# Kernel optimization log

Hardware: AMD Instinct MI355X
Metric: run time of the kernel (lower is better)

Reference implementation:

```python
import jax, jax.numpy as jnp
import numpy as np

B, S = 32, 2048
ENC2 = 1024   # encoder_hidden*2
DEC = 1024    # decoder_hidden
ATT = 1024    # attention_hidden


def setup_inputs() -> dict:
    key = jax.random.key(0)
    ks = jax.random.split(key, 8)
    s_enc = 1.0 / np.sqrt(ENC2)
    s_dec = 1.0 / np.sqrt(DEC)
    s_e = 1.0 / np.sqrt(ATT)
    return {
        "decoder_hidden": jax.random.normal(ks[0], (B, DEC), jnp.float32),
        "encoder_outputs": jax.random.normal(ks[1], (B, S, ENC2), jnp.float32),
        "mask": jnp.ones((B, S), dtype=bool),
        "W_enc": jax.random.uniform(ks[2], (ENC2, ATT), jnp.float32, -s_enc, s_enc),
        "b_enc": jax.random.uniform(ks[3], (ATT,), jnp.float32, -s_enc, s_enc),
        "W_dec": jax.random.uniform(ks[4], (DEC, ATT), jnp.float32, -s_dec, s_dec),
        "b_dec": jax.random.uniform(ks[5], (ATT,), jnp.float32, -s_dec, s_dec),
        "w_e": jax.random.uniform(ks[6], (ATT,), jnp.float32, -s_e, s_e),
        "b_e": jax.random.uniform(ks[7], (), jnp.float32, -s_e, s_e),
    }


def reference(decoder_hidden, encoder_outputs, mask, W_enc, b_enc, W_dec, b_dec, w_e, b_e):
    # encoder_proj: (B, S, ATT)
    encoder_proj = jnp.einsum('bse,ea->bsa', encoder_outputs, W_enc) + b_enc
    # decoder_proj: (B, 1, ATT)
    decoder_proj = (decoder_hidden @ W_dec + b_dec)[:, None, :]
    # energy: (B, S) -- Linear(ATT,1) then squeeze
    energy = jnp.einsum('bsa,a->bs', jnp.tanh(encoder_proj + decoder_proj), w_e) + b_e
    energy = jnp.where(mask, energy, -jnp.inf)
    attention_weights = jax.nn.softmax(energy, axis=1)           # (B, S)
    context = jnp.einsum('bs,bse->be', attention_weights, encoder_outputs)  # (B, ENC2)
    return context, attention_weights
```

## Files before the change

### kernel.cpp

```cpp
#include <hip/hip_runtime.h>
#include <math.h>

#define S_LEN 2048
#define ENC2  1024
#define DEC_H 1024
#define ATT   1024
#define BATCH 32

typedef __attribute__((ext_vector_type(8)))  short short8;
typedef __attribute__((ext_vector_type(16))) float f32x16;

#define DP_OFF (ATT * ENC2 * 2)

__device__ __forceinline__ unsigned short f2bf(float f) {
    unsigned int u = __float_as_uint(f);
    return (unsigned short)((u + 0x7FFFu + ((u >> 16) & 1u)) >> 16);
}

__device__ __forceinline__ float tanh_fast(float x) {
    float ax = fabsf(x);
    float e = __expf(-2.0f * ax);
    float t = (1.0f - e) / (1.0f + e);
    return copysignf(t, x);
}

__global__ void k_pack(const float* __restrict__ W, unsigned short* __restrict__ P) {
    int t  = threadIdx.x;
    int kb = blockIdx.x;
    int nb = blockIdx.y * 4 + (t >> 6);
    int l  = t & 63;
    int n  = nb * 32 + (l & 31);
    int k0 = kb * 16 + ((l >> 5) * 8);
    short8 v;
#pragma unroll
    for (int j = 0; j < 8; ++j)
        v[j] = (short)f2bf(W[(size_t)(k0 + j) * ATT + n]);
    *(short8*)(P + (((size_t)kb * 32 + nb) * 64 + l) * 8) = v;
}

__global__ void k_dproj(const float* __restrict__ dec, const float* __restrict__ Wd,
                        const float* __restrict__ b_dec, const float* __restrict__ b_enc,
                        float* __restrict__ dp) {
    int n = blockIdx.x * 256 + threadIdx.x;
    int b = blockIdx.y;
    float acc = b_dec[n] + b_enc[n];
    const float* dh = dec + b * DEC_H;
#pragma unroll 16
    for (int k = 0; k < DEC_H; ++k)
        acc = fmaf(dh[k], Wd[(size_t)k * ATT + n], acc);
    dp[b * ATT + n] = acc;
}

__launch_bounds__(512, 2)
__global__ void k_energy(const float* __restrict__ enc,
                         const short* __restrict__ BP,
                         const float* __restrict__ dp,
                         const float* __restrict__ w_e,
                         const float* __restrict__ b_e,
                         const int* __restrict__ mask,
                         float* __restrict__ energy)
{
    __shared__ short As[64 * 1024];
    float* e_lds = (float*)As;

    const int tid = threadIdx.x;
    const int r0  = blockIdx.x * 64;
    const int b   = r0 >> 11;

    {
        const float* src = enc + (size_t)r0 * ENC2;
        char* smem = (char*)As;
        for (int u = tid; u < 8192; u += 512) {
            int row = u >> 7, slot = u & 127;
            const float* p = src + (size_t)row * ENC2 + slot * 8;
            float4 f0 = *(const float4*)p;
            float4 f1 = *(const float4*)(p + 4);
            short8 v;
            v[0] = (short)f2bf(f0.x); v[1] = (short)f2bf(f0.y);
            v[2] = (short)f2bf(f0.z); v[3] = (short)f2bf(f0.w);
            v[4] = (short)f2bf(f1.x); v[5] = (short)f2bf(f1.y);
            v[6] = (short)f2bf(f1.z); v[7] = (short)f2bf(f1.w);
            int dst = row * 2048 + ((slot * 16) ^ ((row & 15) << 4));
            *(short8*)(smem + dst) = v;
        }
    }
    __syncthreads();

    const int lane = tid & 63;
    const int wid  = tid >> 6;
    const int col  = lane & 31;
    const int hi   = lane >> 5;
    const int nw   = wid * 128;

    float dv[4], wv[4];
#pragma unroll
    for (int nf = 0; nf < 4; ++nf) {
        int n = nw + nf * 32 + col;
        dv[nf] = dp[b * ATT + n];
        wv[nf] = w_e[n];
    }

    f32x16 acc[2][4] = {};
    const int xr = (col & 15) << 4;
    const char* arow0 = (const char*)As + col * 2048;
    const char* arow1 = (const char*)As + (col + 32) * 2048;

    const char* bp = (const char*)BP + (size_t)(wid * 4) * 1024 + lane * 16;

    short8 b0[4], b1[4];
#pragma unroll
    for (int nf = 0; nf < 4; ++nf) b0[nf] = *(const short8*)(bp + nf * 1024);
#pragma unroll
    for (int nf = 0; nf < 4; ++nf) b1[nf] = *(const short8*)(bp + 32768 + nf * 1024);

    for (int kb = 0; kb < 64; kb += 2) {
        {
            int off = ((kb * 32 + hi * 16) ^ xr);
            short8 a0 = *(const short8*)(arow0 + off);
            short8 a1 = *(const short8*)(arow1 + off);
#pragma unroll
            for (int nf = 0; nf < 4; ++nf) {
                acc[0][nf] = __builtin_amdgcn_mfma_f32_32x32x16_bf16(a0, b0[nf], acc[0][nf], 0, 0, 0);
                acc[1][nf] = __builtin_amdgcn_mfma_f32_32x32x16_bf16(a1, b0[nf], acc[1][nf], 0, 0, 0);
            }
            const char* pf = bp + (size_t)(kb + 2 < 64 ? kb + 2 : kb) * 32768;
#pragma unroll
            for (int nf = 0; nf < 4; ++nf) b0[nf] = *(const short8*)(pf + nf * 1024);
        }
        {
            int off = (((kb + 1) * 32 + hi * 16) ^ xr);
            short8 a0 = *(const short8*)(arow0 + off);
            short8 a1 = *(const short8*)(arow1 + off);
#pragma unroll
            for (int nf = 0; nf < 4; ++nf) {
                acc[0][nf] = __builtin_amdgcn_mfma_f32_32x32x16_bf16(a0, b1[nf], acc[0][nf], 0, 0, 0);
                acc[1][nf] = __builtin_amdgcn_mfma_f32_32x32x16_bf16(a1, b1[nf], acc[1][nf], 0, 0, 0);
            }
            const char* pf = bp + (size_t)(kb + 3 < 64 ? kb + 3 : kb) * 32768;
#pragma unroll
            for (int nf = 0; nf < 4; ++nf) b1[nf] = *(const short8*)(pf + nf * 1024);
        }
    }

    float ep[32];
#pragma unroll
    for (int mf = 0; mf < 2; ++mf)
#pragma unroll
        for (int reg = 0; reg < 16; ++reg) {
            float s = 0.0f;
#pragma unroll
            for (int nf = 0; nf < 4; ++nf)
                s = fmaf(wv[nf], tanh_fast(acc[mf][nf][reg] + dv[nf]), s);
            ep[mf * 16 + reg] = s;
        }

#pragma unroll
    for (int d = 1; d < 32; d <<= 1)
#pragma unroll
        for (int j = 0; j < 32; ++j)
            ep[j] += __shfl_xor(ep[j], d, 64);

    __syncthreads();
    if (tid < 64) e_lds[tid] = 0.0f;
    __syncthreads();

    if (col == 0) {
#pragma unroll
        for (int j = 0; j < 32; ++j) {
            int reg = j & 15;
            int row = (j >> 4) * 32 + (reg & 3) + 8 * (reg >> 2) + 4 * hi;
            atomicAdd(&e_lds[row], ep[j]);
        }
    }
    __syncthreads();

    if (tid < 64) {
        int m = r0 + tid;
        float e = e_lds[tid] + b_e[0];
        if (!mask[m]) e = -INFINITY;
        energy[m] = e;
    }
}

__global__ void k_softmax(float* __restrict__ out) {
    int b = blockIdx.x, tid = threadIdx.x;
    float* ew = out + BATCH * ATT + (size_t)b * S_LEN;
    float v[8];
#pragma unroll
    for (int i = 0; i < 8; ++i) v[i] = ew[i * 256 + tid];
    float m = v[0];
#pragma unroll
    for (int i = 1; i < 8; ++i) m = fmaxf(m, v[i]);
#pragma unroll
    for (int d = 1; d < 64; d <<= 1) m = fmaxf(m, __shfl_xor(m, d, 64));
    __shared__ float red[4], red2[4];
    int w = tid >> 6;
    if ((tid & 63) == 0) red[w] = m;
    __syncthreads();
    m = fmaxf(fmaxf(red[0], red[1]), fmaxf(red[2], red[3]));
    float s = 0.0f;
#pragma unroll
    for (int i = 0; i < 8; ++i) { v[i] = __expf(v[i] - m); s += v[i]; }
#pragma unroll
    for (int d = 1; d < 64; d <<= 1) s += __shfl_xor(s, d, 64);
    if ((tid & 63) == 0) red2[w] = s;
    __syncthreads();
    s = red2[0] + red2[1] + red2[2] + red2[3];
    float inv = 1.0f / s;
#pragma unroll
    for (int i = 0; i < 8; ++i) ew[i * 256 + tid] = v[i] * inv;
    float* ctx = out + (size_t)b * ATT;
#pragma unroll
    for (int i = 0; i < 4; ++i) ctx[i * 256 + tid] = 0.0f;
}

__global__ void k_context(const float* __restrict__ enc, const float* __restrict__ wgt,
                          float* __restrict__ ctx) {
    int sx = blockIdx.x, b = blockIdx.y, tid = threadIdx.x;
    __shared__ float wsh[128];
    if (tid < 128) wsh[tid] = wgt[(size_t)b * S_LEN + sx * 128 + tid];
    __syncthreads();
    const float* ep = enc + ((size_t)b * S_LEN + sx * 128) * ENC2 + tid * 4;
    float ax = 0, ay = 0, az = 0, aw = 0;
#pragma unroll 4
    for (int s = 0; s < 128; ++s) {
        float4 e = *(const float4*)(ep + (size_t)s * ENC2);
        float w = wsh[s];
        ax = fmaf(w, e.x, ax); ay = fmaf(w, e.y, ay);
        az = fmaf(w, e.z, az); aw = fmaf(w, e.w, aw);
    }
    float* c = ctx + (size_t)b * ATT + tid * 4;
    atomicAdd(c + 0, ax); atomicAdd(c + 1, ay);
    atomicAdd(c + 2, az); atomicAdd(c + 3, aw);
}

extern "C" void kernel_launch(void* const* d_in, const int* in_sizes, int n_in,
                              void* d_out, int out_size, void* d_ws, size_t ws_size,
                              hipStream_t stream) {
    (void)in_sizes; (void)n_in; (void)out_size; (void)ws_size;
    const float* dec   = (const float*)d_in[0];
    const float* enc   = (const float*)d_in[1];
    const int*   mask  = (const int*)d_in[2];
    const float* W_enc = (const float*)d_in[3];
    const float* b_enc = (const float*)d_in[4];
    const float* W_dec = (const float*)d_in[5];
    const float* b_dec = (const float*)d_in[6];
    const float* w_e   = (const float*)d_in[7];
    const float* b_e   = (const float*)d_in[8];

    float* out = (float*)d_out;
    unsigned short* BP = (unsigned short*)d_ws;
    float* dp = (float*)((char*)d_ws + DP_OFF);
    float* energy = out + BATCH * ATT;

    k_pack<<<dim3(64, 8), 256, 0, stream>>>(W_enc, BP);
    k_dproj<<<dim3(4, 32), 256, 0, stream>>>(dec, W_dec, b_dec, b_enc, dp);
    k_energy<<<1024, 512, 0, stream>>>(enc, (const short*)BP, dp, w_e, b_e, mask, energy);
    k_softmax<<<32, 256, 0, stream>>>(out);
    k_context<<<dim3(16, 32), 256, 0, stream>>>(enc, energy, out);
}
```

Baseline: 640.8 us.

## Pipeline encoder K-chunks through double-buffered LDS in energy kernel

The energy kernel used to stage a whole 64x1024 bf16 tile in LDS before any MFMA work. Now each block handles 256 rows and streams 64x256 K-chunks through a double buffer, so the global load of the next chunk overlaps MFMAs on the current one, and the grid shrinks to 256 blocks. The decoder-projection loop is split into four independent accumulators, and the context kernel batches eight row loads before its FMAs to raise memory-level parallelism. In exchange, the energy kernel adds more barriers and runs fewer blocks, which may lower occupancy and latency hiding on a GPU with many CUs.

```diff
diff --git a/kernel.cpp b/kernel.cpp
--- a/kernel.cpp
+++ b/kernel.cpp
@@ -43,12 +43,16 @@
                         float* __restrict__ dp) {
     int n = blockIdx.x * 256 + threadIdx.x;
     int b = blockIdx.y;
-    float acc = b_dec[n] + b_enc[n];
     const float* dh = dec + b * DEC_H;
-#pragma unroll 16
-    for (int k = 0; k < DEC_H; ++k)
-        acc = fmaf(dh[k], Wd[(size_t)k * ATT + n], acc);
-    dp[b * ATT + n] = acc;
+    float a0 = 0, a1 = 0, a2 = 0, a3 = 0;
+#pragma unroll 8
+    for (int k = 0; k < DEC_H; k += 4) {
+        a0 = fmaf(dh[k + 0], Wd[(size_t)(k + 0) * ATT + n], a0);
+        a1 = fmaf(dh[k + 1], Wd[(size_t)(k + 1) * ATT + n], a1);
+        a2 = fmaf(dh[k + 2], Wd[(size_t)(k + 2) * ATT + n], a2);
+        a3 = fmaf(dh[k + 3], Wd[(size_t)(k + 3) * ATT + n], a3);
+    }
+    dp[b * ATT + n] = b_dec[n] + b_enc[n] + ((a0 + a1) + (a2 + a3));
 }
 
 __launch_bounds__(512, 2)
@@ -60,125 +64,173 @@
                          const int* __restrict__ mask,
                          float* __restrict__ energy)
 {
-    __shared__ short As[64 * 1024];
-    float* e_lds = (float*)As;
-
-    const int tid = threadIdx.x;
-    const int r0  = blockIdx.x * 64;
-    const int b   = r0 >> 11;
+    __shared__ short As[2][64][256];
+    __shared__ float e_lds[64];
+
+    const int tid    = threadIdx.x;
+    const int bid    = blockIdx.x;
+    const int rowblk = bid * 256;
+    const int b      = rowblk >> 11;
+
+    const int lane = tid & 63;
+    const int wid  = tid >> 6;
+    const int col  = lane & 31;
+    const int hi   = lane >> 5;
+    const int hi16 = hi * 16;
+    const int xr   = (col & 15) << 4;
+
+    const int srow  = tid >> 3;
+    const int schk  = tid & 7;
+    const int sw    = (srow & 15) << 4;
+
+    float dv[4], wv[4];
+#pragma unroll
+    for (int nf = 0; nf < 4; ++nf) {
+        int n = wid * 128 + nf * 32 + col;
+        dv[nf] = dp[b * ATT + n];
+        wv[nf] = w_e[n];
+    }
+
+    const char* bpp = (const char*)BP + (wid << 12) + lane * 16;
+
+    f32x16 acc[2][4];
+#pragma unroll
+    for (int mf = 0; mf < 2; ++mf)
+#pragma unroll
+        for (int nf = 0; nf < 4; ++nf)
+#pragma unroll
+            for (int r = 0; r < 16; ++r) acc[mf][nf][r] = 0.0f;
+
+    short8 bb0[4], bb1[4];
+#pragma unroll
+    for (int nf = 0; nf < 4; ++nf) bb0[nf] = *(const short8*)(bpp + nf * 1024);
+#pragma unroll
+    for (int nf = 0; nf < 4; ++nf) bb1[nf] = *(const short8*)(bpp + 32768 + nf * 1024);
 
     {
-        const float* src = enc + (size_t)r0 * ENC2;
-        char* smem = (char*)As;
-        for (int u = tid; u < 8192; u += 512) {
-            int row = u >> 7, slot = u & 127;
-            const float* p = src + (size_t)row * ENC2 + slot * 8;
-            float4 f0 = *(const float4*)p;
-            float4 f1 = *(const float4*)(p + 4);
+        const float* src = enc + ((size_t)(rowblk + srow) << 10) + schk * 32;
+        float4 f[8];
+#pragma unroll
+        for (int i = 0; i < 8; ++i) f[i] = ((const float4*)src)[i];
+        char* dst = (char*)&As[0][0][0] + srow * 512;
+#pragma unroll
+        for (int j = 0; j < 4; ++j) {
+            float4 f0 = f[2 * j], f1 = f[2 * j + 1];
             short8 v;
             v[0] = (short)f2bf(f0.x); v[1] = (short)f2bf(f0.y);
             v[2] = (short)f2bf(f0.z); v[3] = (short)f2bf(f0.w);
             v[4] = (short)f2bf(f1.x); v[5] = (short)f2bf(f1.y);
             v[6] = (short)f2bf(f1.z); v[7] = (short)f2bf(f1.w);
-            int dst = row * 2048 + ((slot * 16) ^ ((row & 15) << 4));
-            *(short8*)(smem + dst) = v;
-        }
-    }
-    __syncthreads();
-
-    const int lane = tid & 63;
-    const int wid  = tid >> 6;
-    const int col  = lane & 31;
-    const int hi   = lane >> 5;
-    const int nw   = wid * 128;
-
-    float dv[4], wv[4];
-#pragma unroll
-    for (int nf = 0; nf < 4; ++nf) {
-        int n = nw + nf * 32 + col;
-        dv[nf] = dp[b * ATT + n];
-        wv[nf] = w_e[n];
-    }
-
-    f32x16 acc[2][4] = {};
-    const int xr = (col & 15) << 4;
-    const char* arow0 = (const char*)As + col * 2048;
-    const char* arow1 = (const char*)As + (col + 32) * 2048;
-
-    const char* bp = (const char*)BP + (size_t)(wid * 4) * 1024 + lane * 16;
-
-    short8 b0[4], b1[4];
-#pragma unroll
-    for (int nf = 0; nf < 4; ++nf) b0[nf] = *(const short8*)(bp + nf * 1024);
-#pragma unroll
-    for (int nf = 0; nf < 4; ++nf) b1[nf] = *(const short8*)(bp + 32768 + nf * 1024);
-
-    for (int kb = 0; kb < 64; kb += 2) {
-        {
-            int off = ((kb * 32 + hi * 16) ^ xr);
-            short8 a0 = *(const short8*)(arow0 + off);
-            short8 a1 = *(const short8*)(arow1 + off);
-#pragma unroll
-            for (int nf = 0; nf < 4; ++nf) {
-                acc[0][nf] = __builtin_amdgcn_mfma_f32_32x32x16_bf16(a0, b0[nf], acc[0][nf], 0, 0, 0);
-                acc[1][nf] = __builtin_amdgcn_mfma_f32_32x32x16_bf16(a1, b0[nf], acc[1][nf], 0, 0, 0);
-            }
-            const char* pf = bp + (size_t)(kb + 2 < 64 ? kb + 2 : kb) * 32768;
-#pragma unroll
-            for (int nf = 0; nf < 4; ++nf) b0[nf] = *(const short8*)(pf + nf * 1024);
-        }
-        {
-            int off = (((kb + 1) * 32 + hi * 16) ^ xr);
-            short8 a0 = *(const short8*)(arow0 + off);
-            short8 a1 = *(const short8*)(arow1 + off);
-#pragma unroll
-            for (int nf = 0; nf < 4; ++nf) {
-                acc[0][nf] = __builtin_amdgcn_mfma_f32_32x32x16_bf16(a0, b1[nf], acc[0][nf], 0, 0, 0);
-                acc[1][nf] = __builtin_amdgcn_mfma_f32_32x32x16_bf16(a1, b1[nf], acc[1][nf], 0, 0, 0);
-            }
-            const char* pf = bp + (size_t)(kb + 3 < 64 ? kb + 3 : kb) * 32768;
-#pragma unroll
-            for (int nf = 0; nf < 4; ++nf) b1[nf] = *(const short8*)(pf + nf * 1024);
-        }
-    }
-
-    float ep[32];
-#pragma unroll
-    for (int mf = 0; mf < 2; ++mf)
-#pragma unroll
-        for (int reg = 0; reg < 16; ++reg) {
-            float s = 0.0f;
-#pragma unroll
-            for (int nf = 0; nf < 4; ++nf)
-                s = fmaf(wv[nf], tanh_fast(acc[mf][nf][reg] + dv[nf]), s);
-            ep[mf * 16 + reg] = s;
-        }
-
-#pragma unroll
-    for (int d = 1; d < 32; d <<= 1)
-#pragma unroll
-        for (int j = 0; j < 32; ++j)
-            ep[j] += __shfl_xor(ep[j], d, 64);
-
-    __syncthreads();
-    if (tid < 64) e_lds[tid] = 0.0f;
-    __syncthreads();
-
-    if (col == 0) {
-#pragma unroll
-        for (int j = 0; j < 32; ++j) {
-            int reg = j & 15;
-            int row = (j >> 4) * 32 + (reg & 3) + 8 * (reg >> 2) + 4 * hi;
-            atomicAdd(&e_lds[row], ep[j]);
-        }
-    }
-    __syncthreads();
-
-    if (tid < 64) {
-        int m = r0 + tid;
-        float e = e_lds[tid] + b_e[0];
-        if (!mask[m]) e = -INFINITY;
-        energy[m] = e;
+            *(short8*)(dst + ((schk * 64 + j * 16) ^ sw)) = v;
+        }
+        __syncthreads();
+    }
+
+#pragma unroll 1
+    for (int q = 0; q < 16; ++q) {
+        float4 f[8];
+        const bool have = (q < 15);
+        if (have) {
+            const int qq = q + 1;
+            const float* src = enc + ((size_t)(rowblk + ((qq >> 2) << 6) + srow) << 10)
+                                   + ((qq & 3) << 8) + schk * 32;
+#pragma unroll
+            for (int i = 0; i < 8; ++i) f[i] = ((const float4*)src)[i];
+        }
+
+        const char* ab    = (const char*)&As[0][0][0] + ((q & 1) << 15);
+        const char* arow0 = ab + col * 512;
+        const char* arow1 = ab + (col + 32) * 512;
+#pragma unroll
+        for (int t = 0; t < 16; t += 2) {
+            const int kb = (q << 4) + t;
+            {
+                int o0 = (t * 32 + hi16) ^ xr;
+                short8 a0 = *(const short8*)(arow0 + o0);
+                short8 a1 = *(const short8*)(arow1 + o0);
+#pragma unroll
+                for (int nf = 0; nf < 4; ++nf) {
+                    acc[0][nf] = __builtin_amdgcn_mfma_f32_32x32x16_bf16(a0, bb0[nf], acc[0][nf], 0, 0, 0);
+                    acc[1][nf] = __builtin_amdgcn_mfma_f32_32x32x16_bf16(a1, bb0[nf], acc[1][nf], 0, 0, 0);
+                }
+                size_t ro = (size_t)((kb + 2) & 63) << 15;
+#pragma unroll
+                for (int nf = 0; nf < 4; ++nf) bb0[nf] = *(const short8*)(bpp + ro + nf * 1024);
+            }
+            {
+                int o1 = ((t + 1) * 32 + hi16) ^ xr;
+                short8 a0 = *(const short8*)(arow0 + o1);
+                short8 a1 = *(const short8*)(arow1 + o1);
+#pragma unroll
+                for (int nf = 0; nf < 4; ++nf) {
+                    acc[0][nf] = __builtin_amdgcn_mfma_f32_32x32x16_bf16(a0, bb1[nf], acc[0][nf], 0, 0, 0);
+                    acc[1][nf] = __builtin_amdgcn_mfma_f32_32x32x16_bf16(a1, bb1[nf], acc[1][nf], 0, 0, 0);
+                }
+                size_t ro = (size_t)((kb + 3) & 63) << 15;
+#pragma unroll
+                for (int nf = 0; nf < 4; ++nf) bb1[nf] = *(const short8*)(bpp + ro + nf * 1024);
+            }
+        }
+
+        __syncthreads();
+        if (have) {
+            char* dst = (char*)&As[0][0][0] + (((q + 1) & 1) << 15) + srow * 512;
+#pragma unroll
+            for (int j = 0; j < 4; ++j) {
+                float4 f0 = f[2 * j], f1 = f[2 * j + 1];
+                short8 v;
+                v[0] = (short)f2bf(f0.x); v[1] = (short)f2bf(f0.y);
+                v[2] = (short)f2bf(f0.z); v[3] = (short)f2bf(f0.w);
+                v[4] = (short)f2bf(f1.x); v[5] = (short)f2bf(f1.y);
+                v[6] = (short)f2bf(f1.z); v[7] = (short)f2bf(f1.w);
+                *(short8*)(dst + ((schk * 64 + j * 16) ^ sw)) = v;
+            }
+        }
+        __syncthreads();
+
+        if ((q & 3) == 3) {
+            const int r0 = rowblk + ((q >> 2) << 6);
+            float ep[32];
+#pragma unroll
+            for (int mf = 0; mf < 2; ++mf)
+#pragma unroll
+                for (int reg = 0; reg < 16; ++reg) {
+                    float s = 0.0f;
+#pragma unroll
+                    for (int nf = 0; nf < 4; ++nf)
+                        s = fmaf(wv[nf], tanh_fast(acc[mf][nf][reg] + dv[nf]), s);
+                    ep[mf * 16 + reg] = s;
+                }
+#pragma unroll
+            for (int d = 1; d < 32; d <<= 1)
+#pragma unroll
+                for (int j = 0; j < 32; ++j)
+                    ep[j] += __shfl_xor(ep[j], d, 64);
+
+            if (tid < 64) e_lds[tid] = 0.0f;
+            __syncthreads();
+            if (col == 0) {
+#pragma unroll
+                for (int j = 0; j < 32; ++j) {
+                    int reg = j & 15;
+                    int row = (j >> 4) * 32 + (reg & 3) + 8 * (reg >> 2) + 4 * hi;
+                    atomicAdd(&e_lds[row], ep[j]);
+                }
+            }
+            __syncthreads();
+            if (tid < 64) {
+                int m = r0 + tid;
+                float e = e_lds[tid] + b_e[0];
+                if (!mask[m]) e = -INFINITY;
+                energy[m] = e;
+            }
+#pragma unroll
+            for (int mf = 0; mf < 2; ++mf)
+#pragma unroll
+                for (int nf = 0; nf < 4; ++nf)
+#pragma unroll
+                    for (int r = 0; r < 16; ++r) acc[mf][nf][r] = 0.0f;
+        }
     }
 }
 
@@ -222,12 +274,17 @@
     __syncthreads();
     const float* ep = enc + ((size_t)b * S_LEN + sx * 128) * ENC2 + tid * 4;
     float ax = 0, ay = 0, az = 0, aw = 0;
-#pragma unroll 4
-    for (int s = 0; s < 128; ++s) {
-        float4 e = *(const float4*)(ep + (size_t)s * ENC2);
-        float w = wsh[s];
-        ax = fmaf(w, e.x, ax); ay = fmaf(w, e.y, ay);
-        az = fmaf(w, e.z, az); aw = fmaf(w, e.w, aw);
+    for (int s0 = 0; s0 < 128; s0 += 8) {
+        float4 r[8];
+#pragma unroll
+        for (int j = 0; j < 8; ++j)
+            r[j] = *(const float4*)(ep + (size_t)(s0 + j) * ENC2);
+#pragma unroll
+        for (int j = 0; j < 8; ++j) {
+            float w = wsh[s0 + j];
+            ax = fmaf(w, r[j].x, ax); ay = fmaf(w, r[j].y, ay);
+            az = fmaf(w, r[j].z, az); aw = fmaf(w, r[j].w, aw);
+        }
     }
     float* c = ctx + (size_t)b * ATT + tid * 4;
     atomicAdd(c + 0, ax); atomicAdd(c + 1, ay);
@@ -255,7 +312,7 @@
 
     k_pack<<<dim3(64, 8), 256, 0, stream>>>(W_enc, BP);
     k_dproj<<<dim3(4, 32), 256, 0, stream>>>(dec, W_dec, b_dec, b_enc, dp);
-    k_energy<<<1024, 512, 0, stream>>>(enc, (const short*)BP, dp, w_e, b_e, mask, energy);
+    k_energy<<<256, 512, 0, stream>>>(enc, (const short*)BP, dp, w_e, b_e, mask, energy);
     k_softmax<<<32, 256, 0, stream>>>(out);
     k_context<<<dim3(16, 32), 256, 0, stream>>>(enc, energy, out);
 }
```

Result: no change. 632.4 us (-1.3%).

## Split energy GEMM across N quarters with double-buffered K-streamed LDS tiles

Applied to the files above, without the earlier changes.

Restructures the energy kernel. Each 64-row stripe is now handled by four 256-thread blocks, one per quarter of the attention dimension. The encoder rows are streamed in 64-wide K chunks through a double-buffered 16KB LDS tile, replacing the full 128KB tile that had to be staged before any math began. Partial energies are combined with global atomics into a zeroed buffer, and the bias and mask are moved into the softmax kernel. The change also adds a bid swizzle, splits the dproj FMA chains into four accumulators, and doubles the context grid with batched loads. In exchange, each encoder row is read and converted four times, and extra atomics and a memset are added.

```diff
diff --git a/kernel.cpp b/kernel.cpp
--- a/kernel.cpp
+++ b/kernel.cpp
@@ -8,6 +8,7 @@
 #define BATCH 32
 
 typedef __attribute__((ext_vector_type(8)))  short short8;
+typedef __attribute__((ext_vector_type(4)))  short s4;
 typedef __attribute__((ext_vector_type(16))) float f32x16;
 
 #define DP_OFF (ATT * ENC2 * 2)
@@ -43,103 +44,135 @@
                         float* __restrict__ dp) {
     int n = blockIdx.x * 256 + threadIdx.x;
     int b = blockIdx.y;
-    float acc = b_dec[n] + b_enc[n];
     const float* dh = dec + b * DEC_H;
-#pragma unroll 16
-    for (int k = 0; k < DEC_H; ++k)
-        acc = fmaf(dh[k], Wd[(size_t)k * ATT + n], acc);
-    dp[b * ATT + n] = acc;
-}
-
-__launch_bounds__(512, 2)
+    float a0 = 0, a1 = 0, a2 = 0, a3 = 0;
+#pragma unroll 8
+    for (int k = 0; k < DEC_H; k += 4) {
+        a0 = fmaf(dh[k + 0], Wd[(size_t)(k + 0) * ATT + n], a0);
+        a1 = fmaf(dh[k + 1], Wd[(size_t)(k + 1) * ATT + n], a1);
+        a2 = fmaf(dh[k + 2], Wd[(size_t)(k + 2) * ATT + n], a2);
+        a3 = fmaf(dh[k + 3], Wd[(size_t)(k + 3) * ATT + n], a3);
+    }
+    dp[b * ATT + n] = b_dec[n] + b_enc[n] + ((a0 + a1) + (a2 + a3));
+}
+
+__launch_bounds__(256, 4)
 __global__ void k_energy(const float* __restrict__ enc,
                          const short* __restrict__ BP,
                          const float* __restrict__ dp,
                          const float* __restrict__ w_e,
-                         const float* __restrict__ b_e,
-                         const int* __restrict__ mask,
-                         float* __restrict__ energy)
+                         float* __restrict__ ew)
 {
-    __shared__ short As[64 * 1024];
-    float* e_lds = (float*)As;
-
-    const int tid = threadIdx.x;
-    const int r0  = blockIdx.x * 64;
-    const int b   = r0 >> 11;
-
-    {
-        const float* src = enc + (size_t)r0 * ENC2;
-        char* smem = (char*)As;
-        for (int u = tid; u < 8192; u += 512) {
-            int row = u >> 7, slot = u & 127;
-            const float* p = src + (size_t)row * ENC2 + slot * 8;
-            float4 f0 = *(const float4*)p;
-            float4 f1 = *(const float4*)(p + 4);
-            short8 v;
-            v[0] = (short)f2bf(f0.x); v[1] = (short)f2bf(f0.y);
-            v[2] = (short)f2bf(f0.z); v[3] = (short)f2bf(f0.w);
-            v[4] = (short)f2bf(f1.x); v[5] = (short)f2bf(f1.y);
-            v[6] = (short)f2bf(f1.z); v[7] = (short)f2bf(f1.w);
-            int dst = row * 2048 + ((slot * 16) ^ ((row & 15) << 4));
-            *(short8*)(smem + dst) = v;
-        }
-    }
-    __syncthreads();
+    __shared__ short As[2][64][64];
+    __shared__ float e_lds[64];
+
+    const int tid   = threadIdx.x;
+    const int bid   = blockIdx.x;
+    const int swz   = (bid & 7) * 512 + (bid >> 3);
+    const int stripe = swz >> 2;
+    const int nq    = swz & 3;
+    const int r0    = stripe << 6;
+    const int b     = stripe >> 5;
 
     const int lane = tid & 63;
     const int wid  = tid >> 6;
     const int col  = lane & 31;
     const int hi   = lane >> 5;
-    const int nw   = wid * 128;
-
-    float dv[4], wv[4];
-#pragma unroll
-    for (int nf = 0; nf < 4; ++nf) {
-        int n = nw + nf * 32 + col;
+    const int hi16 = hi << 4;
+    const int xr   = (col & 7) << 4;
+
+    float dv[2], wv[2];
+#pragma unroll
+    for (int nf = 0; nf < 2; ++nf) {
+        int n = nq * 256 + wid * 64 + nf * 32 + col;
         dv[nf] = dp[b * ATT + n];
         wv[nf] = w_e[n];
     }
 
-    f32x16 acc[2][4] = {};
-    const int xr = (col & 15) << 4;
-    const char* arow0 = (const char*)As + col * 2048;
-    const char* arow1 = (const char*)As + (col + 32) * 2048;
-
-    const char* bp = (const char*)BP + (size_t)(wid * 4) * 1024 + lane * 16;
-
-    short8 b0[4], b1[4];
-#pragma unroll
-    for (int nf = 0; nf < 4; ++nf) b0[nf] = *(const short8*)(bp + nf * 1024);
-#pragma unroll
-    for (int nf = 0; nf < 4; ++nf) b1[nf] = *(const short8*)(bp + 32768 + nf * 1024);
-
-    for (int kb = 0; kb < 64; kb += 2) {
-        {
-            int off = ((kb * 32 + hi * 16) ^ xr);
-            short8 a0 = *(const short8*)(arow0 + off);
-            short8 a1 = *(const short8*)(arow1 + off);
-#pragma unroll
-            for (int nf = 0; nf < 4; ++nf) {
-                acc[0][nf] = __builtin_amdgcn_mfma_f32_32x32x16_bf16(a0, b0[nf], acc[0][nf], 0, 0, 0);
-                acc[1][nf] = __builtin_amdgcn_mfma_f32_32x32x16_bf16(a1, b0[nf], acc[1][nf], 0, 0, 0);
-            }
-            const char* pf = bp + (size_t)(kb + 2 < 64 ? kb + 2 : kb) * 32768;
-#pragma unroll
-            for (int nf = 0; nf < 4; ++nf) b0[nf] = *(const short8*)(pf + nf * 1024);
-        }
-        {
-            int off = (((kb + 1) * 32 + hi * 16) ^ xr);
-            short8 a0 = *(const short8*)(arow0 + off);
-            short8 a1 = *(const short8*)(arow1 + off);
-#pragma unroll
-            for (int nf = 0; nf < 4; ++nf) {
-                acc[0][nf] = __builtin_amdgcn_mfma_f32_32x32x16_bf16(a0, b1[nf], acc[0][nf], 0, 0, 0);
-                acc[1][nf] = __builtin_amdgcn_mfma_f32_32x32x16_bf16(a1, b1[nf], acc[1][nf], 0, 0, 0);
-            }
-            const char* pf = bp + (size_t)(kb + 3 < 64 ? kb + 3 : kb) * 32768;
-#pragma unroll
-            for (int nf = 0; nf < 4; ++nf) b1[nf] = *(const short8*)(pf + nf * 1024);
-        }
+    const char* bpp = (const char*)BP + (size_t)(nq * 8 + wid * 2) * 1024 + lane * 16;
+
+    f32x16 acc[2][2];
+#pragma unroll
+    for (int mf = 0; mf < 2; ++mf)
+#pragma unroll
+        for (int nf = 0; nf < 2; ++nf)
+#pragma unroll
+            for (int r = 0; r < 16; ++r) acc[mf][nf][r] = 0.0f;
+
+    short8 bb0[2], bb1[2];
+    bb0[0] = *(const short8*)(bpp);
+    bb0[1] = *(const short8*)(bpp + 1024);
+    bb1[0] = *(const short8*)(bpp + 32768);
+    bb1[1] = *(const short8*)(bpp + 32768 + 1024);
+
+#pragma unroll
+    for (int i = 0; i < 4; ++i) {
+        int u = i * 256 + tid, row = u >> 4, fs = u & 15;
+        float4 fv = *(const float4*)(enc + ((size_t)(r0 + row) << 10) + (fs << 2));
+        s4 v; v[0] = (short)f2bf(fv.x); v[1] = (short)f2bf(fv.y);
+              v[2] = (short)f2bf(fv.z); v[3] = (short)f2bf(fv.w);
+        *(s4*)((char*)As + row * 128 + ((fs * 8) ^ ((row & 7) << 4))) = v;
+    }
+    __syncthreads();
+
+#pragma unroll 1
+    for (int ph = 0; ph < 16; ++ph) {
+        float4 f[4];
+        const bool have = (ph < 15);
+        if (have) {
+#pragma unroll
+            for (int i = 0; i < 4; ++i) {
+                int u = i * 256 + tid, row = u >> 4, fs = u & 15;
+                f[i] = *(const float4*)(enc + ((size_t)(r0 + row) << 10)
+                                            + ((ph + 1) << 6) + (fs << 2));
+            }
+        }
+
+        const char* ab    = (const char*)As + ((ph & 1) << 13);
+        const char* arow0 = ab + col * 128;
+        const char* arow1 = ab + (col + 32) * 128;
+        const int kbase = ph << 2;
+#pragma unroll
+        for (int t = 0; t < 4; t += 2) {
+            {
+                int off = ((t << 5) + hi16) ^ xr;
+                short8 a0 = *(const short8*)(arow0 + off);
+                short8 a1 = *(const short8*)(arow1 + off);
+                acc[0][0] = __builtin_amdgcn_mfma_f32_32x32x16_bf16(a0, bb0[0], acc[0][0], 0, 0, 0);
+                acc[0][1] = __builtin_amdgcn_mfma_f32_32x32x16_bf16(a0, bb0[1], acc[0][1], 0, 0, 0);
+                acc[1][0] = __builtin_amdgcn_mfma_f32_32x32x16_bf16(a1, bb0[0], acc[1][0], 0, 0, 0);
+                acc[1][1] = __builtin_amdgcn_mfma_f32_32x32x16_bf16(a1, bb0[1], acc[1][1], 0, 0, 0);
+                size_t ro = (size_t)((kbase + t + 2) & 63) << 15;
+                bb0[0] = *(const short8*)(bpp + ro);
+                bb0[1] = *(const short8*)(bpp + ro + 1024);
+            }
+            {
+                int off = (((t + 1) << 5) + hi16) ^ xr;
+                short8 a0 = *(const short8*)(arow0 + off);
+                short8 a1 = *(const short8*)(arow1 + off);
+                acc[0][0] = __builtin_amdgcn_mfma_f32_32x32x16_bf16(a0, bb1[0], acc[0][0], 0, 0, 0);
+                acc[0][1] = __builtin_amdgcn_mfma_f32_32x32x16_bf16(a0, bb1[1], acc[0][1], 0, 0, 0);
+                acc[1][0] = __builtin_amdgcn_mfma_f32_32x32x16_bf16(a1, bb1[0], acc[1][0], 0, 0, 0);
+                acc[1][1] = __builtin_amdgcn_mfma_f32_32x32x16_bf16(a1, bb1[1], acc[1][1], 0, 0, 0);
+                size_t ro = (size_t)((kbase + t + 3) & 63) << 15;
+                bb1[0] = *(const short8*)(bpp + ro);
+                bb1[1] = *(const short8*)(bpp + ro + 1024);
+            }
+        }
+
+        __syncthreads();
+        if (have) {
+            char* dst = (char*)As + (((ph + 1) & 1) << 13);
+#pragma unroll
+            for (int i = 0; i < 4; ++i) {
+                int u = i * 256 + tid, row = u >> 4, fs = u & 15;
+                float4 fv = f[i];
+                s4 v; v[0] = (short)f2bf(fv.x); v[1] = (short)f2bf(fv.y);
+                      v[2] = (short)f2bf(fv.z); v[3] = (short)f2bf(fv.w);
+                *(s4*)(dst + row * 128 + ((fs * 8) ^ ((row & 7) << 4))) = v;
+            }
+        }
+        __syncthreads();
     }
 
     float ep[32];
@@ -147,23 +180,18 @@
     for (int mf = 0; mf < 2; ++mf)
 #pragma unroll
         for (int reg = 0; reg < 16; ++reg) {
-            float s = 0.0f;
-#pragma unroll
-            for (int nf = 0; nf < 4; ++nf)
-                s = fmaf(wv[nf], tanh_fast(acc[mf][nf][reg] + dv[nf]), s);
+            float s = fmaf(wv[0], tanh_fast(acc[mf][0][reg] + dv[0]),
+                           wv[1] * tanh_fast(acc[mf][1][reg] + dv[1]));
             ep[mf * 16 + reg] = s;
         }
-
 #pragma unroll
     for (int d = 1; d < 32; d <<= 1)
 #pragma unroll
         for (int j = 0; j < 32; ++j)
             ep[j] += __shfl_xor(ep[j], d, 64);
 
-    __syncthreads();
     if (tid < 64) e_lds[tid] = 0.0f;
     __syncthreads();
-
     if (col == 0) {
 #pragma unroll
         for (int j = 0; j < 32; ++j) {
@@ -173,21 +201,22 @@
         }
     }
     __syncthreads();
-
-    if (tid < 64) {
-        int m = r0 + tid;
-        float e = e_lds[tid] + b_e[0];
-        if (!mask[m]) e = -INFINITY;
-        energy[m] = e;
-    }
-}
-
-__global__ void k_softmax(float* __restrict__ out) {
+    if (tid < 64) atomicAdd(&ew[r0 + tid], e_lds[tid]);
+}
+
+__global__ void k_softmax(const int* __restrict__ mask, const float* __restrict__ b_e,
+                          float* __restrict__ out) {
     int b = blockIdx.x, tid = threadIdx.x;
     float* ew = out + BATCH * ATT + (size_t)b * S_LEN;
+    const int* mk = mask + (size_t)b * S_LEN;
+    float be = b_e[0];
     float v[8];
 #pragma unroll
-    for (int i = 0; i < 8; ++i) v[i] = ew[i * 256 + tid];
+    for (int i = 0; i < 8; ++i) {
+        int s = i * 256 + tid;
+        float e = ew[s] + be;
+        v[i] = mk[s] ? e : -INFINITY;
+    }
     float m = v[0];
 #pragma unroll
     for (int i = 1; i < 8; ++i) m = fmaxf(m, v[i]);
@@ -217,17 +246,22 @@
 __global__ void k_context(const float* __restrict__ enc, const float* __restrict__ wgt,
                           float* __restrict__ ctx) {
     int sx = blockIdx.x, b = blockIdx.y, tid = threadIdx.x;
-    __shared__ float wsh[128];
-    if (tid < 128) wsh[tid] = wgt[(size_t)b * S_LEN + sx * 128 + tid];
-    __syncthreads();
-    const float* ep = enc + ((size_t)b * S_LEN + sx * 128) * ENC2 + tid * 4;
+    __shared__ float wsh[64];
+    if (tid < 64) wsh[tid] = wgt[(size_t)b * S_LEN + sx * 64 + tid];
+    __syncthreads();
+    const float* ep = enc + ((size_t)b * S_LEN + sx * 64) * ENC2 + tid * 4;
     float ax = 0, ay = 0, az = 0, aw = 0;
-#pragma unroll 4
-    for (int s = 0; s < 128; ++s) {
-        float4 e = *(const float4*)(ep + (size_t)s * ENC2);
-        float w = wsh[s];
-        ax = fmaf(w, e.x, ax); ay = fmaf(w, e.y, ay);
-        az = fmaf(w, e.z, az); aw = fmaf(w, e.w, aw);
+    for (int s0 = 0; s0 < 64; s0 += 8) {
+        float4 r[8];
+#pragma unroll
+        for (int j = 0; j < 8; ++j)
+            r[j] = *(const float4*)(ep + (size_t)(s0 + j) * ENC2);
+#pragma unroll
+        for (int j = 0; j < 8; ++j) {
+            float w = wsh[s0 + j];
+            ax = fmaf(w, r[j].x, ax); ay = fmaf(w, r[j].y, ay);
+            az = fmaf(w, r[j].z, az); aw = fmaf(w, r[j].w, aw);
+        }
     }
     float* c = ctx + (size_t)b * ATT + tid * 4;
     atomicAdd(c + 0, ax); atomicAdd(c + 1, ay);
@@ -251,11 +285,12 @@
     float* out = (float*)d_out;
     unsigned short* BP = (unsigned short*)d_ws;
     float* dp = (float*)((char*)d_ws + DP_OFF);
-    float* energy = out + BATCH * ATT;
-
+    float* ew = out + BATCH * ATT;
+
+    hipMemsetAsync(ew, 0, (size_t)BATCH * S_LEN * sizeof(float), stream);
     k_pack<<<dim3(64, 8), 256, 0, stream>>>(W_enc, BP);
     k_dproj<<<dim3(4, 32), 256, 0, stream>>>(dec, W_dec, b_dec, b_enc, dp);
-    k_energy<<<1024, 512, 0, stream>>>(enc, (const short*)BP, dp, w_e, b_e, mask, energy);
-    k_softmax<<<32, 256, 0, stream>>>(out);
-    k_context<<<dim3(16, 32), 256, 0, stream>>>(enc, energy, out);
-}
+    k_energy<<<4096, 256, 0, stream>>>(enc, (const short*)BP, dp, w_e, ew);
+    k_softmax<<<32, 256, 0, stream>>>(mask, b_e, out);
+    k_context<<<dim3(32, 32), 256, 0, stream>>>(enc, ew, out);
+}
```

Result: faster. 574.1 us (-10.4%).
